# Optimization experiments

Hardware: AMD Instinct MI355X
Metric: run time of the kernel (lower is better)

The kernel has to match this reference:

```python
import jax, jax.numpy as jnp
import numpy as np

N = 4096
K = 64
E = N * K
LD = 2      # location_dim
ED = 8      # attention embed_dim
H = 256     # lck_structure width
BN_EPS = 1e-5


def setup_inputs() -> dict:
    key = jax.random.key(0)
    ks = jax.random.split(key, 12)
    coor = jax.random.normal(ks[0], (E, 2 * LD), dtype=jnp.float32)
    row = jnp.repeat(jnp.arange(N, dtype=jnp.int64), K)
    col = jax.random.randint(ks[1], (E,), 0, N, dtype=jnp.int64)
    sparse_idx = jnp.stack([row, col], axis=0)
    geodesic = jax.random.uniform(ks[2], (N, N), dtype=jnp.float32)
    angle_ratio = jax.random.uniform(ks[3], (N, N), dtype=jnp.float32)
    # LocalConditionalKer params: Linear(4,H), Linear(H,H), BN(H), Linear(H,1)
    W0 = jax.random.normal(ks[4], (2 * LD, H), dtype=jnp.float32) / np.sqrt(2 * LD)
    b0 = jnp.zeros((H,), jnp.float32)
    W1 = jax.random.normal(ks[5], (H, H), dtype=jnp.float32) / np.sqrt(H)
    b1 = jnp.zeros((H,), jnp.float32)
    gamma = jnp.ones((H,), jnp.float32)
    beta = jnp.zeros((H,), jnp.float32)
    W2 = jax.random.normal(ks[6], (H, 1), dtype=jnp.float32) / np.sqrt(H)
    b2 = jnp.zeros((1,), jnp.float32)
    # Attention params: query/key Linear(LD, ED)
    Wq = jax.random.normal(ks[7], (LD, ED), dtype=jnp.float32) / np.sqrt(LD)
    bq = jnp.zeros((ED,), jnp.float32)
    Wk = jax.random.normal(ks[8], (LD, ED), dtype=jnp.float32) / np.sqrt(LD)
    bk = jnp.zeros((ED,), jnp.float32)
    x = jax.random.normal(ks[9], (1,), dtype=jnp.float32)
    return dict(x=x, coor=coor, sparse_idx=sparse_idx, geodesic=geodesic,
                angle_ratio=angle_ratio, W0=W0, b0=b0, W1=W1, b1=b1,
                gamma=gamma, beta=beta, W2=W2, b2=b2,
                Wq=Wq, bq=bq, Wk=Wk, bk=bk)


def _lck(coor, W0, b0, W1, b1, gamma, beta, W2, b2):
    # loop semantics: activation applied before every layer except j==1
    h = jnp.tanh(coor) @ W0 + b0          # j=0: Linear(4,H)
    h = h @ W1 + b1                        # j=1: Linear(H,H), no pre-activation
    h = jnp.tanh(h)                        # j=2: BN(H) in training mode (batch stats)
    mu = jnp.mean(h, axis=0)
    var = jnp.var(h, axis=0)               # biased variance, as torch BN uses
    h = gamma * (h - mu) * jax.lax.rsqrt(var + BN_EPS) + beta
    h = jnp.tanh(h) @ W2 + b2              # j=3: Linear(H,1)
    return jax.nn.relu(h)                  # [E,1]


def reference(x, coor, sparse_idx, geodesic, angle_ratio,
              W0, b0, W1, b1, gamma, beta, W2, b2, Wq, bq, Wk, bk):
    row, col = sparse_idx[0], sparse_idx[1]
    # per-edge kernel value, scattered into dense NxN (duplicates summed)
    vals = _lck(coor, W0, b0, W1, b1, gamma, beta, W2, b2).reshape(-1)  # [E]
    lcker = jnp.zeros((N, N), vals.dtype).at[row, col].add(vals)
    # attention over neighbors
    sphere = coor[:, :LD] + coor[:, LD:]           # [E, 2]
    sphere = sphere.reshape(N, K, LD)               # [N, K, 2]
    center = sphere[:, :1, :]                       # [N, 1, 2]
    q = center @ Wq + bq                            # [N, 1, ED]
    k = sphere @ Wk + bk                            # [N, K, ED]
    att = jnp.abs(jnp.einsum('nqe,nke->nqk', q, k).squeeze(1))  # [N, K]
    alpha = jnp.zeros((N, N), att.dtype).at[row, col].add(att.reshape(-1))
    distance_decay = jnp.exp(-alpha * geodesic)
    return lcker * distance_decay * angle_ratio
```

## Files before the change

kernel.cpp:

```cpp
#include <hip/hip_runtime.h>

#define N_ 4096
#define K_ 64
#define E_ (N_*K_)
#define H_ 256
#define EPS_ 1e-5f
#define L2E_ 1.4426950408889634f
#define TL2E_ 2.8853900817779268f

#if __has_builtin(__builtin_amdgcn_exp2f)
#define EXP2(x) __builtin_amdgcn_exp2f(x)
#else
#define EXP2(x) __expf((x) * 0.6931471805599453f)
#endif

__device__ __forceinline__ float ftanh(float x) {
    float e = EXP2(x * TL2E_);
    return 1.0f - 2.0f * __builtin_amdgcn_rcpf(e + 1.0f);
}

__global__ __launch_bounds__(256) void prep_kernel(
    const float* __restrict__ W0, const float* __restrict__ b0,
    const float* __restrict__ W1, const float* __restrict__ b1,
    const float* __restrict__ W2, const float* __restrict__ b2,
    float* __restrict__ W01g, float* __restrict__ swp, float* __restrict__ sums)
{
    int c = threadIdx.x;
    float a0 = 0.f, a1 = 0.f, a2 = 0.f, a3 = 0.f, ab = 0.f;
    #pragma unroll 8
    for (int h = 0; h < H_; ++h) {
        float w = W1[h * H_ + c];
        a0 = fmaf(W0[h], w, a0);
        a1 = fmaf(W0[H_ + h], w, a1);
        a2 = fmaf(W0[2 * H_ + h], w, a2);
        a3 = fmaf(W0[3 * H_ + h], w, a3);
        ab = fmaf(b0[h], w, ab);
    }
    W01g[c]          = TL2E_ * a0;
    W01g[H_ + c]     = TL2E_ * a1;
    W01g[2 * H_ + c] = TL2E_ * a2;
    W01g[3 * H_ + c] = TL2E_ * a3;
    W01g[4 * H_ + c] = TL2E_ * (ab + b1[c]);
    sums[c] = 0.f;
    sums[H_ + c] = 0.f;

    __shared__ float red[256];
    red[c] = W2[c];
    __syncthreads();
    for (int s = 128; s > 0; s >>= 1) {
        if (c < s) red[c] += red[c + s];
        __syncthreads();
    }
    if (c == 0) swp[0] = red[0] + b2[0];
}

__global__ __launch_bounds__(256, 8) void stats_kernel(
    const float* __restrict__ coor, const float* __restrict__ W01g,
    float* __restrict__ part)
{
    const int c = threadIdx.x;
    const float w0 = W01g[c],          w1 = W01g[H_ + c];
    const float w2 = W01g[2 * H_ + c], w3 = W01g[3 * H_ + c];
    const float bb = W01g[4 * H_ + c];
    __shared__ float4 T[128];
    const int e0 = blockIdx.x * 128;
    if (c < 128) {
        float4 v = reinterpret_cast<const float4*>(coor)[e0 + c];
        T[c] = make_float4(ftanh(v.x), ftanh(v.y), ftanh(v.z), ftanh(v.w));
    }
    __syncthreads();
    float sr = 0.f, sr2 = 0.f;
    #pragma unroll 8
    for (int i = 0; i < 128; ++i) {
        float4 t = T[i];
        float u = fmaf(t.w, w3, fmaf(t.z, w2, fmaf(t.y, w1, fmaf(t.x, w0, bb))));
        float r = __builtin_amdgcn_rcpf(EXP2(u) + 1.0f);
        sr += r;
        sr2 = fmaf(r, r, sr2);
    }
    part[blockIdx.x * 512 + c] = sr;
    part[blockIdx.x * 512 + 256 + c] = sr2;
}

__global__ __launch_bounds__(512) void reduce_kernel(
    const float* __restrict__ part, float* __restrict__ sums)
{
    int t = threadIdx.x;
    int b0 = blockIdx.x * 64;
    float local = 0.f;
    #pragma unroll 8
    for (int b = b0; b < b0 + 64; ++b) local += part[b * 512 + t];
    atomicAdd(&sums[t], local);
}

__global__ __launch_bounds__(256, 8) void edge_kernel(
    const float* __restrict__ coor, const int* __restrict__ idx,
    const float* __restrict__ sums, const float* __restrict__ W01g,
    const float* __restrict__ gamma, const float* __restrict__ beta,
    const float* __restrict__ W2, const float* __restrict__ swp,
    const float* __restrict__ Wq, const float* __restrict__ bq,
    const float* __restrict__ Wk, const float* __restrict__ bk,
    const float* __restrict__ geo, const float* __restrict__ ang,
    float* __restrict__ out)
{
    __shared__ float4 FS[2 * H_];
    __shared__ float4 TS[128];
    __shared__ float2 EXY[128];
    __shared__ float  ACC[8][128];

    const int t = threadIdx.x;
    const int row0 = blockIdx.x * 2;

    {
        const float inv = 1.0f / (float)E_;
        float sp = sums[t] * inv;
        float sq = sums[H_ + t] * inv;
        float mu = 1.0f - 2.0f * sp;
        float var = 4.0f * fmaf(-sp, sp, sq);
        float a  = gamma[t] * rsqrtf(var + EPS_);
        float bf = fmaf(-mu, a, beta[t]);
        FS[2 * t]     = make_float4(W01g[t], W01g[H_ + t], W01g[2 * H_ + t], W01g[3 * H_ + t]);
        FS[2 * t + 1] = make_float4(W01g[4 * H_ + t], -4.0f * L2E_ * a,
                                    TL2E_ * (a + bf), -2.0f * W2[t]);
    }
    int col = 0;
    if (t < 128) {
        float4 ce = reinterpret_cast<const float4*>(coor)[row0 * K_ + t];
        TS[t] = make_float4(ftanh(ce.x), ftanh(ce.y), ftanh(ce.z), ftanh(ce.w));
        EXY[t] = make_float2(ce.x + ce.z, ce.y + ce.w);
        col = idx[E_ + row0 * K_ + t];
    }
    __syncthreads();

    {
        float4 z = make_float4(0.f, 0.f, 0.f, 0.f);
        float4* orow = reinterpret_cast<float4*>(out + (size_t)row0 * N_);
        #pragma unroll
        for (int i = 0; i < 8; ++i) orow[i * 256 + t] = z;
    }
    size_t p = 0;
    float g = 0.f, an = 0.f;
    if (t < 128) {
        p = (size_t)(row0 + (t >> 6)) * N_ + col;
        g = geo[p];
        an = ang[p];
    }

    const int eg = (t & 31) * 4;
    const int chunk = t >> 5;
    const float4 tq0 = TS[eg], tq1 = TS[eg + 1], tq2 = TS[eg + 2], tq3 = TS[eg + 3];
    const float4* Fp = &FS[chunk * 64];
    float a0 = 0.f, a1 = 0.f, a2 = 0.f, a3 = 0.f;
    #pragma unroll 4
    for (int i = 0; i < 32; ++i) {
        float4 f0 = Fp[2 * i];
        float4 f1 = Fp[2 * i + 1];
        #define EVAL(tq, ak) { \
            float u = fmaf(tq.w, f0.w, fmaf(tq.z, f0.z, fmaf(tq.y, f0.y, fmaf(tq.x, f0.x, f1.x)))); \
            float r = __builtin_amdgcn_rcpf(EXP2(u) + 1.0f); \
            float r2 = __builtin_amdgcn_rcpf(EXP2(fmaf(r, f1.y, f1.z)) + 1.0f); \
            ak = fmaf(r2, f1.w, ak); }
        EVAL(tq0, a0) EVAL(tq1, a1) EVAL(tq2, a2) EVAL(tq3, a3)
        #undef EVAL
    }
    *reinterpret_cast<float4*>(&ACC[chunk][eg]) = make_float4(a0, a1, a2, a3);
    __syncthreads();

    const int w = t >> 6, lane = t & 63;
    if (w < 2) {
        const int eb = t;
        float val = swp[0];
        #pragma unroll
        for (int c = 0; c < 8; ++c) val += ACC[c][eb];
        val = fmaxf(val, 0.f);

        float2 exy = EXY[eb];
        float ex = exy.x, ey = exy.y;
        float sx = __shfl(ex, 0), sy = __shfl(ey, 0);
        float att = 0.f;
        #pragma unroll
        for (int j = 0; j < 8; ++j) {
            float qj = fmaf(sy, Wq[8 + j], fmaf(sx, Wq[j], bq[j]));
            float kj = fmaf(ey, Wk[8 + j], fmaf(ex, Wk[j], bk[j]));
            att = fmaf(qj, kj, att);
        }
        att = fabsf(att);

        float vsum = val, asum = att;
        bool leader = true;
        for (int j = 0; j < 64; ++j) {
            int   bc = __shfl(col, j);
            float bv = __shfl(val, j);
            float ba = __shfl(att, j);
            if (bc == col && j != lane) {
                if (j < lane) leader = false;
                else { vsum += bv; asum += ba; }
            }
        }
        if (leader) {
            out[p] = vsum * __expf(-asum * g) * an;
        }
    }
}

extern "C" void kernel_launch(void* const* d_in, const int* in_sizes, int n_in,
                              void* d_out, int out_size, void* d_ws, size_t ws_size,
                              hipStream_t stream)
{
    const float* coor  = (const float*)d_in[1];
    const int*   idx   = (const int*)d_in[2];
    const float* geo   = (const float*)d_in[3];
    const float* ang   = (const float*)d_in[4];
    const float* W0    = (const float*)d_in[5];
    const float* b0    = (const float*)d_in[6];
    const float* W1    = (const float*)d_in[7];
    const float* b1    = (const float*)d_in[8];
    const float* gamma = (const float*)d_in[9];
    const float* beta  = (const float*)d_in[10];
    const float* W2    = (const float*)d_in[11];
    const float* b2    = (const float*)d_in[12];
    const float* Wq    = (const float*)d_in[13];
    const float* bq    = (const float*)d_in[14];
    const float* Wk    = (const float*)d_in[15];
    const float* bk    = (const float*)d_in[16];

    float* ws   = (float*)d_ws;
    float* swp  = ws;
    float* sums = ws + 256;
    float* W01g = ws + 1024;
    float* part = ws + 4096;

    prep_kernel<<<1, 256, 0, stream>>>(W0, b0, W1, b1, W2, b2, W01g, swp, sums);
    stats_kernel<<<E_ / 128, 256, 0, stream>>>(coor, W01g, part);
    reduce_kernel<<<32, 512, 0, stream>>>(part, sums);
    edge_kernel<<<N_ / 2, 256, 0, stream>>>(coor, idx, sums, W01g, gamma, beta,
                                            W2, swp, Wq, bq, Wk, bk, geo, ang,
                                            (float*)d_out);
}
```

Measured before the change: 84.50 us.

## Split attention and duplicate detection into a separate precompute kernel

A new att_kernel computes per-edge attention, finds duplicate columns with a 64-step shuffle scan, gathers geodesic and angle values and stores the decay factor, packed position and a duplicate mask per edge. The edge kernel then only sums values over the mask bits with a ffs-driven shuffle loop instead of the full 64-iteration shuffle scan, and moves the output zeroing ahead of the barrier. The aim is to take the random gathers and the duplicate scan off the MLP-heavy edge kernel's critical path. In exchange it adds an extra launch and about 4 MB of workspace traffic. Leader detection uses De != 0, so a leader whose decay underflows to zero skips its store, which leaves the zero already written.

```diff
diff --git a/kernel.cpp b/kernel.cpp
--- a/kernel.cpp
+++ b/kernel.cpp
@@ -17,6 +17,57 @@
 __device__ __forceinline__ float ftanh(float x) {
     float e = EXP2(x * TL2E_);
     return 1.0f - 2.0f * __builtin_amdgcn_rcpf(e + 1.0f);
+}
+
+__global__ __launch_bounds__(256, 8) void att_kernel(
+    const float* __restrict__ coor, const int* __restrict__ idx,
+    const float* __restrict__ geo, const float* __restrict__ ang,
+    const float* __restrict__ Wq, const float* __restrict__ bq,
+    const float* __restrict__ Wk, const float* __restrict__ bk,
+    float* __restrict__ D, unsigned int* __restrict__ P,
+    unsigned long long* __restrict__ M)
+{
+    const int t = threadIdx.x;
+    const int e = blockIdx.x * 256 + t;
+    const int lane = t & 63;
+    const int row = e >> 6;
+    const int col = idx[E_ + e];
+
+    float4 ce = reinterpret_cast<const float4*>(coor)[e];
+    float ex = ce.x + ce.z, ey = ce.y + ce.w;
+    float sx = __shfl(ex, 0), sy = __shfl(ey, 0);
+    float att = 0.f;
+    #pragma unroll
+    for (int j = 0; j < 8; ++j) {
+        float qj = fmaf(sy, Wq[8 + j], fmaf(sx, Wq[j], bq[j]));
+        float kj = fmaf(ey, Wk[8 + j], fmaf(ex, Wk[j], bk[j]));
+        att = fmaf(qj, kj, att);
+    }
+    att = fabsf(att);
+
+    unsigned long long m = 0;
+    float asum = att;
+    bool leader = true;
+    for (int j = 0; j < 64; ++j) {
+        int   bc = __shfl(col, j);
+        float ba = __shfl(att, j);
+        bool match = (bc == col);
+        if (match) {
+            m |= (1ull << j);
+            if (j < lane) leader = false;
+            if (j != lane) asum += ba;
+        }
+    }
+
+    unsigned int p = ((unsigned)row << 12) | (unsigned)col;
+    float d = 0.f;
+    if (leader) {
+        size_t pp = (size_t)row * N_ + col;
+        d = __expf(-asum * geo[pp]) * ang[pp];
+    }
+    D[e] = d;
+    P[e] = p;
+    M[e] = leader ? m : 0ull;
 }
 
 __global__ __launch_bounds__(256) void prep_kernel(
@@ -94,22 +145,21 @@
 }
 
 __global__ __launch_bounds__(256, 8) void edge_kernel(
-    const float* __restrict__ coor, const int* __restrict__ idx,
+    const float* __restrict__ coor,
     const float* __restrict__ sums, const float* __restrict__ W01g,
     const float* __restrict__ gamma, const float* __restrict__ beta,
     const float* __restrict__ W2, const float* __restrict__ swp,
-    const float* __restrict__ Wq, const float* __restrict__ bq,
-    const float* __restrict__ Wk, const float* __restrict__ bk,
-    const float* __restrict__ geo, const float* __restrict__ ang,
+    const float* __restrict__ D, const unsigned int* __restrict__ P,
+    const unsigned long long* __restrict__ M,
     float* __restrict__ out)
 {
     __shared__ float4 FS[2 * H_];
     __shared__ float4 TS[128];
-    __shared__ float2 EXY[128];
     __shared__ float  ACC[8][128];
 
     const int t = threadIdx.x;
     const int row0 = blockIdx.x * 2;
+    const int eb0 = blockIdx.x * 128;
 
     {
         const float inv = 1.0f / (float)E_;
@@ -123,28 +173,23 @@
         FS[2 * t + 1] = make_float4(W01g[4 * H_ + t], -4.0f * L2E_ * a,
                                     TL2E_ * (a + bf), -2.0f * W2[t]);
     }
-    int col = 0;
+    float De = 0.f;
+    unsigned int Pe = 0;
+    unsigned long long Me = 0;
     if (t < 128) {
-        float4 ce = reinterpret_cast<const float4*>(coor)[row0 * K_ + t];
+        float4 ce = reinterpret_cast<const float4*>(coor)[eb0 + t];
         TS[t] = make_float4(ftanh(ce.x), ftanh(ce.y), ftanh(ce.z), ftanh(ce.w));
-        EXY[t] = make_float2(ce.x + ce.z, ce.y + ce.w);
-        col = idx[E_ + row0 * K_ + t];
-    }
-    __syncthreads();
-
+        De = D[eb0 + t];
+        Pe = P[eb0 + t];
+        Me = M[eb0 + t];
+    }
     {
         float4 z = make_float4(0.f, 0.f, 0.f, 0.f);
         float4* orow = reinterpret_cast<float4*>(out + (size_t)row0 * N_);
         #pragma unroll
         for (int i = 0; i < 8; ++i) orow[i * 256 + t] = z;
     }
-    size_t p = 0;
-    float g = 0.f, an = 0.f;
-    if (t < 128) {
-        p = (size_t)(row0 + (t >> 6)) * N_ + col;
-        g = geo[p];
-        an = ang[p];
-    }
+    __syncthreads();
 
     const int eg = (t & 31) * 4;
     const int chunk = t >> 5;
@@ -168,38 +213,20 @@
 
     const int w = t >> 6, lane = t & 63;
     if (w < 2) {
-        const int eb = t;
         float val = swp[0];
         #pragma unroll
-        for (int c = 0; c < 8; ++c) val += ACC[c][eb];
+        for (int c = 0; c < 8; ++c) val += ACC[c][t];
         val = fmaxf(val, 0.f);
 
-        float2 exy = EXY[eb];
-        float ex = exy.x, ey = exy.y;
-        float sx = __shfl(ex, 0), sy = __shfl(ey, 0);
-        float att = 0.f;
-        #pragma unroll
-        for (int j = 0; j < 8; ++j) {
-            float qj = fmaf(sy, Wq[8 + j], fmaf(sx, Wq[j], bq[j]));
-            float kj = fmaf(ey, Wk[8 + j], fmaf(ex, Wk[j], bk[j]));
-            att = fmaf(qj, kj, att);
+        float vsum = val;
+        unsigned long long m2 = Me & ~(1ull << lane);
+        while (__any(m2 != 0ull)) {
+            unsigned long long pick = m2 ? m2 : 1ull;
+            int j = __ffsll((unsigned long long)pick) - 1;
+            float bv = __shfl(val, j);
+            if (m2) { vsum += bv; m2 &= m2 - 1; }
         }
-        att = fabsf(att);
-
-        float vsum = val, asum = att;
-        bool leader = true;
-        for (int j = 0; j < 64; ++j) {
-            int   bc = __shfl(col, j);
-            float bv = __shfl(val, j);
-            float ba = __shfl(att, j);
-            if (bc == col && j != lane) {
-                if (j < lane) leader = false;
-                else { vsum += bv; asum += ba; }
-            }
-        }
-        if (leader) {
-            out[p] = vsum * __expf(-asum * g) * an;
-        }
+        if (De != 0.f) out[Pe] = vsum * De;
     }
 }
 
@@ -224,16 +251,20 @@
     const float* Wk    = (const float*)d_in[15];
     const float* bk    = (const float*)d_in[16];
 
-    float* ws   = (float*)d_ws;
-    float* swp  = ws;
-    float* sums = ws + 256;
-    float* W01g = ws + 1024;
-    float* part = ws + 4096;
-
+    char* ws = (char*)d_ws;
+    float*              swp  = (float*)ws;
+    float*              sums = (float*)(ws + 1024);
+    float*              W01g = (float*)(ws + 4096);
+    float*              D    = (float*)(ws + 16384);
+    unsigned int*       P    = (unsigned int*)(ws + 16384 + (size_t)E_*4);
+    unsigned long long* M    = (unsigned long long*)(ws + 16384 + (size_t)E_*8);
+    float*              part = (float*)(ws + 16384 + (size_t)E_*16);
+
+    att_kernel<<<E_ / 256, 256, 0, stream>>>(coor, idx, geo, ang, Wq, bq, Wk, bk,
+                                             D, P, M);
     prep_kernel<<<1, 256, 0, stream>>>(W0, b0, W1, b1, W2, b2, W01g, swp, sums);
     stats_kernel<<<E_ / 128, 256, 0, stream>>>(coor, W01g, part);
     reduce_kernel<<<32, 512, 0, stream>>>(part, sums);
-    edge_kernel<<<N_ / 2, 256, 0, stream>>>(coor, idx, sums, W01g, gamma, beta,
-                                            W2, swp, Wq, bq, Wk, bk, geo, ang,
-                                            (float*)d_out);
-}
+    edge_kernel<<<N_ / 2, 256, 0, stream>>>(coor, sums, W01g, gamma, beta, W2,
+                                            swp, D, P, M, (float*)d_out);
+}
```

Result: slower. 93.65 us (+10.8%).

## Hoist BN folding into finalize kernel and speed up duplicate-column merge

Applied to the files above, without the earlier changes.

Moves the per-block BatchNorm statistics folding into a single-block finalize kernel, so each edge block just loads the precomputed coefficient table. The attention score is now computed while the edge coordinates load. Duplicate-column detection uses LDS-vectorised comparisons that build a bitmask, replacing the 64-iteration shuffle loop, and the geo/ang gathers are issued only by leader lanes. This cuts redundant per-block arithmetic and shuffle work, at the cost of one extra kernel launch and later gather latency.

```diff
diff --git a/kernel.cpp b/kernel.cpp
--- a/kernel.cpp
+++ b/kernel.cpp
@@ -93,11 +93,32 @@
     atomicAdd(&sums[t], local);
 }
 
+__global__ __launch_bounds__(256) void finalize_kernel(
+    const float* __restrict__ sums, const float* __restrict__ gamma,
+    const float* __restrict__ beta, const float* __restrict__ W2,
+    const float* __restrict__ W01g, float* __restrict__ folded)
+{
+    int c = threadIdx.x;
+    const float inv = 1.0f / (float)E_;
+    float sp = sums[c] * inv;
+    float sq = sums[256 + c] * inv;
+    float mu = 1.0f - 2.0f * sp;
+    float var = 4.0f * fmaf(-sp, sp, sq);
+    float a  = gamma[c] * rsqrtf(var + EPS_);
+    float bf = fmaf(-mu, a, beta[c]);
+    folded[8 * c + 0] = W01g[c];
+    folded[8 * c + 1] = W01g[H_ + c];
+    folded[8 * c + 2] = W01g[2 * H_ + c];
+    folded[8 * c + 3] = W01g[3 * H_ + c];
+    folded[8 * c + 4] = W01g[4 * H_ + c];
+    folded[8 * c + 5] = -4.0f * L2E_ * a;
+    folded[8 * c + 6] = TL2E_ * (a + bf);
+    folded[8 * c + 7] = -2.0f * W2[c];
+}
+
 __global__ __launch_bounds__(256, 8) void edge_kernel(
     const float* __restrict__ coor, const int* __restrict__ idx,
-    const float* __restrict__ sums, const float* __restrict__ W01g,
-    const float* __restrict__ gamma, const float* __restrict__ beta,
-    const float* __restrict__ W2, const float* __restrict__ swp,
+    const float* __restrict__ folded, const float* __restrict__ swp,
     const float* __restrict__ Wq, const float* __restrict__ bq,
     const float* __restrict__ Wk, const float* __restrict__ bk,
     const float* __restrict__ geo, const float* __restrict__ ang,
@@ -105,46 +126,44 @@
 {
     __shared__ float4 FS[2 * H_];
     __shared__ float4 TS[128];
-    __shared__ float2 EXY[128];
     __shared__ float  ACC[8][128];
+    __shared__ int    COL[128];
+    __shared__ float  ATT[128];
 
     const int t = threadIdx.x;
     const int row0 = blockIdx.x * 2;
+    const int eb0 = blockIdx.x * 128;
 
     {
-        const float inv = 1.0f / (float)E_;
-        float sp = sums[t] * inv;
-        float sq = sums[H_ + t] * inv;
-        float mu = 1.0f - 2.0f * sp;
-        float var = 4.0f * fmaf(-sp, sp, sq);
-        float a  = gamma[t] * rsqrtf(var + EPS_);
-        float bf = fmaf(-mu, a, beta[t]);
-        FS[2 * t]     = make_float4(W01g[t], W01g[H_ + t], W01g[2 * H_ + t], W01g[3 * H_ + t]);
-        FS[2 * t + 1] = make_float4(W01g[4 * H_ + t], -4.0f * L2E_ * a,
-                                    TL2E_ * (a + bf), -2.0f * W2[t]);
+        const float4* F = reinterpret_cast<const float4*>(folded);
+        FS[t] = F[t];
+        FS[t + 256] = F[t + 256];
     }
     int col = 0;
+    float att = 0.f;
     if (t < 128) {
-        float4 ce = reinterpret_cast<const float4*>(coor)[row0 * K_ + t];
+        float4 ce = reinterpret_cast<const float4*>(coor)[eb0 + t];
         TS[t] = make_float4(ftanh(ce.x), ftanh(ce.y), ftanh(ce.z), ftanh(ce.w));
-        EXY[t] = make_float2(ce.x + ce.z, ce.y + ce.w);
-        col = idx[E_ + row0 * K_ + t];
-    }
-    __syncthreads();
-
+        col = idx[E_ + eb0 + t];
+        float ex = ce.x + ce.z, ey = ce.y + ce.w;
+        float sx = __shfl(ex, 0), sy = __shfl(ey, 0);
+        #pragma unroll
+        for (int j = 0; j < 8; ++j) {
+            float qj = fmaf(sy, Wq[8 + j], fmaf(sx, Wq[j], bq[j]));
+            float kj = fmaf(ey, Wk[8 + j], fmaf(ex, Wk[j], bk[j]));
+            att = fmaf(qj, kj, att);
+        }
+        att = fabsf(att);
+        COL[t] = col;
+        ATT[t] = att;
+    }
     {
         float4 z = make_float4(0.f, 0.f, 0.f, 0.f);
         float4* orow = reinterpret_cast<float4*>(out + (size_t)row0 * N_);
         #pragma unroll
         for (int i = 0; i < 8; ++i) orow[i * 256 + t] = z;
     }
-    size_t p = 0;
-    float g = 0.f, an = 0.f;
-    if (t < 128) {
-        p = (size_t)(row0 + (t >> 6)) * N_ + col;
-        g = geo[p];
-        an = ang[p];
-    }
+    __syncthreads();
 
     const int eg = (t & 31) * 4;
     const int chunk = t >> 5;
@@ -168,37 +187,40 @@
 
     const int w = t >> 6, lane = t & 63;
     if (w < 2) {
-        const int eb = t;
         float val = swp[0];
         #pragma unroll
-        for (int c = 0; c < 8; ++c) val += ACC[c][eb];
+        for (int c = 0; c < 8; ++c) val += ACC[c][t];
         val = fmaxf(val, 0.f);
 
-        float2 exy = EXY[eb];
-        float ex = exy.x, ey = exy.y;
-        float sx = __shfl(ex, 0), sy = __shfl(ey, 0);
-        float att = 0.f;
-        #pragma unroll
-        for (int j = 0; j < 8; ++j) {
-            float qj = fmaf(sy, Wq[8 + j], fmaf(sx, Wq[j], bq[j]));
-            float kj = fmaf(ey, Wk[8 + j], fmaf(ex, Wk[j], bk[j]));
-            att = fmaf(qj, kj, att);
-        }
-        att = fabsf(att);
-
-        float vsum = val, asum = att;
-        bool leader = true;
-        for (int j = 0; j < 64; ++j) {
-            int   bc = __shfl(col, j);
+        const int rb = w * 64;
+        unsigned long long m = 0;
+        float asum = 0.f;
+        #pragma unroll 8
+        for (int j4 = 0; j4 < 16; ++j4) {
+            int4   c4 = *reinterpret_cast<const int4*>(&COL[rb + 4 * j4]);
+            float4 a4 = *reinterpret_cast<const float4*>(&ATT[rb + 4 * j4]);
+            m |= (unsigned long long)(c4.x == col) << (4 * j4 + 0);
+            m |= (unsigned long long)(c4.y == col) << (4 * j4 + 1);
+            m |= (unsigned long long)(c4.z == col) << (4 * j4 + 2);
+            m |= (unsigned long long)(c4.w == col) << (4 * j4 + 3);
+            asum += (c4.x == col) ? a4.x : 0.f;
+            asum += (c4.y == col) ? a4.y : 0.f;
+            asum += (c4.z == col) ? a4.z : 0.f;
+            asum += (c4.w == col) ? a4.w : 0.f;
+        }
+        bool leader = ((m & ((1ull << lane) - 1ull)) == 0ull);
+
+        float vsum = val;
+        unsigned long long m2 = m & ~(1ull << lane);
+        while (__any(m2 != 0ull)) {
+            unsigned long long pick = m2 ? m2 : 1ull;
+            int j = __ffsll(pick) - 1;
             float bv = __shfl(val, j);
-            float ba = __shfl(att, j);
-            if (bc == col && j != lane) {
-                if (j < lane) leader = false;
-                else { vsum += bv; asum += ba; }
-            }
+            if (m2) { vsum += bv; m2 &= m2 - 1; }
         }
         if (leader) {
-            out[p] = vsum * __expf(-asum * g) * an;
+            size_t p = (size_t)(row0 + w) * N_ + col;
+            out[p] = vsum * __expf(-asum * geo[p]) * ang[p];
         }
     }
 }
@@ -224,16 +246,17 @@
     const float* Wk    = (const float*)d_in[15];
     const float* bk    = (const float*)d_in[16];
 
-    float* ws   = (float*)d_ws;
-    float* swp  = ws;
-    float* sums = ws + 256;
-    float* W01g = ws + 1024;
-    float* part = ws + 4096;
+    char* ws = (char*)d_ws;
+    float* swp    = (float*)ws;
+    float* sums   = (float*)(ws + 1024);
+    float* W01g   = (float*)(ws + 4096);
+    float* folded = (float*)(ws + 10240);
+    float* part   = (float*)(ws + 20480);
 
     prep_kernel<<<1, 256, 0, stream>>>(W0, b0, W1, b1, W2, b2, W01g, swp, sums);
     stats_kernel<<<E_ / 128, 256, 0, stream>>>(coor, W01g, part);
     reduce_kernel<<<32, 512, 0, stream>>>(part, sums);
-    edge_kernel<<<N_ / 2, 256, 0, stream>>>(coor, idx, sums, W01g, gamma, beta,
-                                            W2, swp, Wq, bq, Wk, bk, geo, ang,
-                                            (float*)d_out);
-}
+    finalize_kernel<<<1, 256, 0, stream>>>(sums, gamma, beta, W2, W01g, folded);
+    edge_kernel<<<N_ / 2, 256, 0, stream>>>(coor, idx, folded, swp,
+                                            Wq, bq, Wk, bk, geo, ang, (float*)d_out);
+}
```

After: 84.31 us. About the same (-0.2%).
